# Optimization experiments

Measured on AMD Instinct MI355X. Metric: run time of the kernel, lower is better.

Reference implementation:

```python
import jax, jax.numpy as jnp
import numpy as np


def setup_inputs() -> dict:
    key = jax.random.key(0)
    ks = jax.random.split(key, 6)
    b, t, s, qu, vu, d = 8, 64, 512, 512, 512, 512
    return {
        "query": jax.random.normal(ks[0], (b, t, qu), jnp.float32),
        "value": jax.random.normal(ks[1], (b, s, vu), jnp.float32),
        "mask": jax.random.randint(ks[2], (b, s), 0, 2).astype(bool),
        "W1_w": jax.random.normal(ks[3], (qu, d), jnp.float32) * (1.0 / np.sqrt(qu)),
        "W1_b": jnp.zeros((d,), jnp.float32),
        "W2_w": jax.random.normal(ks[4], (vu, d), jnp.float32) * (1.0 / np.sqrt(vu)),
        "W2_b": jnp.zeros((d,), jnp.float32),
        "scale": jax.random.normal(ks[5], (d,), jnp.float32) * 0.05,
    }


def reference(query, value, mask, W1_w, W1_b, W2_w, W2_b, scale):
    # Dense projections
    q = jnp.einsum('btq,qd->btd', query, W1_w) + W1_b   # [b,t,d]
    k = jnp.einsum('bsv,vd->bsd', value, W2_w) + W2_b   # [b,s,d]
    # Additive (Bahdanau) score with learned scale vector (Keras use_scale=True)
    # scores[b,t,s] = sum_d scale[d] * tanh(q[b,t,d] + k[b,s,d])
    scores = jnp.einsum('btsd,d->bts', jnp.tanh(q[:, :, None, :] + k[:, None, :, :]), scale)
    # Mask over source positions (value mask); query mask is all-ones (no-op)
    scores = jnp.where(mask[:, None, :], scores, jnp.float32(-1e9))
    attention_weights = jax.nn.softmax(scores, axis=-1)   # [b,t,s]
    context_vector = jnp.einsum('bts,bsv->btv', attention_weights, value)  # [b,t,vu]
    return context_vector, attention_weights
```

## Files before the change

kernel.cpp:

```cpp
#include <hip/hip_runtime.h>
#include <hip/hip_bf16.h>

#define B_  8
#define T_  64
#define S_  512
#define D_  512

#define QN (512 * 512)
#define KN (4096 * 512)

#define TLOG2E 2.8853900817779268f
#define LOG2E  1.4426950408889634f

typedef __attribute__((ext_vector_type(8))) short bf16x8;
typedef __attribute__((ext_vector_type(4))) float f32x4;

__device__ __forceinline__ unsigned int pk2(float a, float b) {
    float2 f; f.x = a; f.y = b;
    __hip_bfloat162 h = __float22bfloat162_rn(f);
    return *(unsigned int*)&h;
}
#define BF2X(U) __uint_as_float((U) << 16)
#define BF2Y(U) __uint_as_float((U) & 0xffff0000u)

__global__ __launch_bounds__(256) void mfma_gemm(
    const float* __restrict__ query, const float* __restrict__ value,
    const float* __restrict__ W1, const float* __restrict__ W2,
    const float* __restrict__ b1, const float* __restrict__ b2,
    float* __restrict__ qproj, unsigned short* __restrict__ kTb)
{
    __shared__ __align__(16) unsigned short Ab[2][64][72];
    __shared__ __align__(16) unsigned short Bs[2][64][72];

    const int x = blockIdx.x;
    const float *A, *W;
    int tm, tn;
    bool isq;
    if (x < 512) {
        tm = (x & 7) * 8 + ((x >> 3) & 7);
        tn = x >> 6;
        A = value; W = W2; isq = false;
    } else {
        int r = x - 512;
        tm = r >> 3; tn = r & 7;
        A = query; W = W1; isq = true;
    }

    const int tid  = threadIdx.x;
    const int lane = tid & 63;
    const int wid  = tid >> 6;
    const int wm = (wid & 1) * 32, wn = (wid >> 1) * 32;
    const int fm = lane & 15, fq = lane >> 4;

    f32x4 acc00 = {0.f, 0.f, 0.f, 0.f};
    f32x4 acc01 = acc00, acc10 = acc00, acc11 = acc00;

    const int ar = tid >> 2;
    const int kc = (tid & 3) * 16;
    const float* Ag = A + (size_t)(tm * 64 + ar) * 512 + kc;
    const int c0 = (tid & 15) * 4;
    const int kp = (tid >> 4) * 2;
    const float* Wg = W + (size_t)kp * 512 + tn * 64 + c0;

    float4 av0, av1, av2, av3;
    float4 wv0, wv1, wv2, wv3;

#define LOADT(KOFF) do {                                                      \
        av0 = *(const float4*)(Ag + (KOFF));                                  \
        av1 = *(const float4*)(Ag + (KOFF) + 4);                              \
        av2 = *(const float4*)(Ag + (KOFF) + 8);                              \
        av3 = *(const float4*)(Ag + (KOFF) + 12);                             \
        wv0 = *(const float4*)(Wg + (size_t)(KOFF) * 512);                    \
        wv1 = *(const float4*)(Wg + (size_t)(KOFF) * 512 + 512);              \
        wv2 = *(const float4*)(Wg + (size_t)((KOFF) + 32) * 512);             \
        wv3 = *(const float4*)(Wg + (size_t)((KOFF) + 32) * 512 + 512);       \
    } while (0)

#define STAGE(BUF) do {                                                       \
        uint4 p0, p1;                                                         \
        p0.x = pk2(av0.x, av0.y); p0.y = pk2(av0.z, av0.w);                   \
        p0.z = pk2(av1.x, av1.y); p0.w = pk2(av1.z, av1.w);                   \
        p1.x = pk2(av2.x, av2.y); p1.y = pk2(av2.z, av2.w);                   \
        p1.z = pk2(av3.x, av3.y); p1.w = pk2(av3.z, av3.w);                   \
        *(uint4*)&Ab[BUF][ar][kc]     = p0;                                   \
        *(uint4*)&Ab[BUF][ar][kc + 8] = p1;                                   \
        *(unsigned int*)&Bs[BUF][c0 + 0][kp]      = pk2(wv0.x, wv1.x);        \
        *(unsigned int*)&Bs[BUF][c0 + 1][kp]      = pk2(wv0.y, wv1.y);        \
        *(unsigned int*)&Bs[BUF][c0 + 2][kp]      = pk2(wv0.z, wv1.z);        \
        *(unsigned int*)&Bs[BUF][c0 + 3][kp]      = pk2(wv0.w, wv1.w);        \
        *(unsigned int*)&Bs[BUF][c0 + 0][kp + 32] = pk2(wv2.x, wv3.x);        \
        *(unsigned int*)&Bs[BUF][c0 + 1][kp + 32] = pk2(wv2.y, wv3.y);        \
        *(unsigned int*)&Bs[BUF][c0 + 2][kp + 32] = pk2(wv2.z, wv3.z);        \
        *(unsigned int*)&Bs[BUF][c0 + 3][kp + 32] = pk2(wv2.w, wv3.w);        \
    } while (0)

    LOADT(0);
    STAGE(0);
    LOADT(64);
    __syncthreads();

    for (int i = 0; i < 8; ++i) {
        const int cur = i & 1, nxt = cur ^ 1;
        bf16x8 a0, a1, b0, b1v;
#pragma unroll
        for (int kk = 0; kk < 64; kk += 32) {
            a0  = *(const bf16x8*)&Ab[cur][wm + fm][kk + fq * 8];
            a1  = *(const bf16x8*)&Ab[cur][wm + 16 + fm][kk + fq * 8];
            b0  = *(const bf16x8*)&Bs[cur][wn + fm][kk + fq * 8];
            b1v = *(const bf16x8*)&Bs[cur][wn + 16 + fm][kk + fq * 8];
            acc00 = __builtin_amdgcn_mfma_f32_16x16x32_bf16(a0, b0,  acc00, 0, 0, 0);
            acc01 = __builtin_amdgcn_mfma_f32_16x16x32_bf16(a0, b1v, acc01, 0, 0, 0);
            acc10 = __builtin_amdgcn_mfma_f32_16x16x32_bf16(a1, b0,  acc10, 0, 0, 0);
            acc11 = __builtin_amdgcn_mfma_f32_16x16x32_bf16(a1, b1v, acc11, 0, 0, 0);
        }
        if (i < 7) {
            STAGE(nxt);
            const int kn = ((i + 2) & 7) * 64;
            LOADT(kn);
        }
        __syncthreads();
    }
#undef STAGE
#undef LOADT

    const int n0 = tn * 64 + wn + fm;
    const int n1 = n0 + 16;
    const int m0 = tm * 64 + wm + fq * 4;
    if (isq) {
        float bias0 = b1[n0] + b2[n0];
        float bias1 = b1[n1] + b2[n1];
#pragma unroll
        for (int r = 0; r < 4; ++r) {
            qproj[(size_t)(m0 + r) * 512 + n0]      = (acc00[r] + bias0) * TLOG2E;
            qproj[(size_t)(m0 + r) * 512 + n1]      = (acc01[r] + bias1) * TLOG2E;
            qproj[(size_t)(m0 + 16 + r) * 512 + n0] = (acc10[r] + bias0) * TLOG2E;
            qproj[(size_t)(m0 + 16 + r) * 512 + n1] = (acc11[r] + bias1) * TLOG2E;
        }
    } else {
        const int bb = m0 >> 9;
        const int sl = m0 & 511;
        unsigned short* kb = kTb + (size_t)(bb * 512) * 512;
        uint2 o;
        o.x = pk2(acc00[0] * TLOG2E, acc00[1] * TLOG2E);
        o.y = pk2(acc00[2] * TLOG2E, acc00[3] * TLOG2E);
        *(uint2*)(kb + (size_t)n0 * 512 + sl) = o;
        o.x = pk2(acc10[0] * TLOG2E, acc10[1] * TLOG2E);
        o.y = pk2(acc10[2] * TLOG2E, acc10[3] * TLOG2E);
        *(uint2*)(kb + (size_t)n0 * 512 + sl + 16) = o;
        o.x = pk2(acc01[0] * TLOG2E, acc01[1] * TLOG2E);
        o.y = pk2(acc01[2] * TLOG2E, acc01[3] * TLOG2E);
        *(uint2*)(kb + (size_t)n1 * 512 + sl) = o;
        o.x = pk2(acc11[0] * TLOG2E, acc11[1] * TLOG2E);
        o.y = pk2(acc11[2] * TLOG2E, acc11[3] * TLOG2E);
        *(uint2*)(kb + (size_t)n1 * 512 + sl + 16) = o;
    }
}

__global__ __launch_bounds__(1024) void fused_attn(
    const float* __restrict__ qproj, const unsigned short* __restrict__ kTb,
    const int*   __restrict__ mask,  const float* __restrict__ scale,
    const float* __restrict__ value,
    float* __restrict__ ctx, float* __restrict__ attn)
{
    const int blk = blockIdx.x;
    const int b  = blk & 7;
    const int tp = blk >> 3;
    const size_t row0 = (size_t)(b * T_ + tp * 2);

    __shared__ __align__(16) float q0A[512];
    __shared__ __align__(16) float dA[512];
    __shared__ __align__(16) float cA[512];
    __shared__ __align__(16) float4 pex[4][256];
    __shared__ __align__(16) float2 wp2[512];
    __shared__ __align__(16) float4 part[2][8][128];
    __shared__ float2 red2[16];

    const int tid  = threadIdx.x;
    const int lane = tid & 63;
    const int wid  = tid >> 6;

    if (tid < 512) {
        float q0v = qproj[row0 * D_ + tid];
        float q1v = qproj[(row0 + 1) * D_ + tid];
        q0A[tid] = q0v;
        dA[tid]  = __builtin_amdgcn_exp2f(q1v - q0v);
        cA[tid]  = scale[tid];
    }
    __syncthreads();

    const int sp  = tid & 255;
    const int dq  = tid >> 8;
    const int dlo = dq * 128;
    const unsigned short* kb = kTb + ((size_t)(b * 512 + dlo)) * 512 + sp * 2;

    float p00 = 0.f, p10 = 0.f, p01 = 0.f, p11 = 0.f;

    unsigned int nf0 = *(const unsigned int*)(kb);
    unsigned int nf1 = *(const unsigned int*)(kb + 512);
    unsigned int nf2 = *(const unsigned int*)(kb + 1024);
    unsigned int nf3 = *(const unsigned int*)(kb + 1536);

#define SC2(KU, QV, DV, CV) do {                                              \
        float e0 = __builtin_amdgcn_exp2f((QV) + BF2X(KU));                   \
        float ra = __builtin_amdgcn_rcpf(e0 + 1.0f);                          \
        float rb = __builtin_amdgcn_rcpf(fmaf(e0, (DV), 1.0f));               \
        p00 = fmaf((CV), ra, p00); p10 = fmaf((CV), rb, p10);                 \
        float e1 = __builtin_amdgcn_exp2f((QV) + BF2Y(KU));                   \
        float rc = __builtin_amdgcn_rcpf(e1 + 1.0f);                          \
        float rd = __builtin_amdgcn_rcpf(fmaf(e1, (DV), 1.0f));               \
        p01 = fmaf((CV), rc, p01); p11 = fmaf((CV), rd, p11);                 \
    } while (0)

    for (int g = 0; g < 32; ++g) {
        unsigned int kf0 = nf0, kf1 = nf1, kf2 = nf2, kf3 = nf3;
        const unsigned short* nb = kb + (size_t)(((g + 1) & 31) * 4) * 512;
        nf0 = *(const unsigned int*)(nb);
        nf1 = *(const unsigned int*)(nb + 512);
        nf2 = *(const unsigned int*)(nb + 1024);
        nf3 = *(const unsigned int*)(nb + 1536);
        const int d0 = dlo + g * 4;
        float4 q4 = *(const float4*)&q0A[d0];
        float4 dl = *(const float4*)&dA[d0];
        float4 c4 = *(const float4*)&cA[d0];
        SC2(kf0, q4.x, dl.x, c4.x);
        SC2(kf1, q4.y, dl.y, c4.y);
        SC2(kf2, q4.z, dl.z, c4.z);
        SC2(kf3, q4.w, dl.w, c4.w);
    }
#undef SC2

    {
        float4 pq; pq.x = p00; pq.y = p10; pq.z = p01; pq.w = p11;
        pex[dq][sp] = pq;
    }
    __syncthreads();

    float x0 = 0.f, x1 = 0.f;
    if (tid < 512) {
        const int s = tid;
        const int s2 = s >> 1;
        const bool odd = (s & 1) != 0;
        float4 r0 = pex[0][s2], r1 = pex[1][s2];
        float4 r2 = pex[2][s2], r3 = pex[3][s2];
        float pt0 = odd ? ((r0.z + r1.z) + (r2.z + r3.z))
                        : ((r0.x + r1.x) + (r2.x + r3.x));
        float pt1 = odd ? ((r0.w + r1.w) + (r2.w + r3.w))
                        : ((r0.y + r1.y) + (r2.y + r3.y));
        const int m = mask[b * S_ + s];
        x0 = m ? (-2.0f * pt0) : -1e9f;
        x1 = m ? (-2.0f * pt1) : -1e9f;
        float2 mx; mx.x = x0; mx.y = x1;
#pragma unroll
        for (int off = 32; off >= 1; off >>= 1) {
            mx.x = fmaxf(mx.x, __shfl_xor(mx.x, off));
            mx.y = fmaxf(mx.y, __shfl_xor(mx.y, off));
        }
        if (lane == 0) red2[wid] = mx;
    }
    __syncthreads();

    float e0 = 0.f, e1 = 0.f;
    if (tid < 512) {
        float2 M = red2[0];
#pragma unroll
        for (int i = 1; i < 8; ++i) {
            M.x = fmaxf(M.x, red2[i].x);
            M.y = fmaxf(M.y, red2[i].y);
        }
        e0 = __builtin_amdgcn_exp2f((x0 - M.x) * LOG2E);
        e1 = __builtin_amdgcn_exp2f((x1 - M.y) * LOG2E);
        float2 sm; sm.x = e0; sm.y = e1;
#pragma unroll
        for (int off = 32; off >= 1; off >>= 1) {
            sm.x += __shfl_xor(sm.x, off);
            sm.y += __shfl_xor(sm.y, off);
        }
        if (lane == 0) red2[8 + wid] = sm;
    }
    __syncthreads();

    if (tid < 512) {
        const int s = tid;
        float2 SS = red2[8];
#pragma unroll
        for (int i = 9; i < 16; ++i) {
            SS.x += red2[i].x;
            SS.y += red2[i].y;
        }
        const float w0 = e0 * __builtin_amdgcn_rcpf(SS.x);
        const float w1 = e1 * __builtin_amdgcn_rcpf(SS.y);
        float2 wpair; wpair.x = w0; wpair.y = w1;
        wp2[s] = wpair;
        attn[row0 * S_ + s]       = w0;
        attn[(row0 + 1) * S_ + s] = w1;
    }
    __syncthreads();

    const int g  = tid >> 7;
    const int v4 = tid & 127;
    const float* vb = value + ((size_t)(b * S_) + g * 64) * D_ + v4 * 4;
    float4 a0; a0.x = 0.f; a0.y = 0.f; a0.z = 0.f; a0.w = 0.f;
    float4 a1 = a0;
#pragma unroll 4
    for (int i = 0; i < 64; ++i) {
        float4 vv = *(const float4*)(vb + (size_t)i * D_);
        float2 w = wp2[g * 64 + i];
        a0.x = fmaf(w.x, vv.x, a0.x); a0.y = fmaf(w.x, vv.y, a0.y);
        a0.z = fmaf(w.x, vv.z, a0.z); a0.w = fmaf(w.x, vv.w, a0.w);
        a1.x = fmaf(w.y, vv.x, a1.x); a1.y = fmaf(w.y, vv.y, a1.y);
        a1.z = fmaf(w.y, vv.z, a1.z); a1.w = fmaf(w.y, vv.w, a1.w);
    }
    part[0][g][v4] = a0;
    part[1][g][v4] = a1;
    __syncthreads();
    if (tid < 256) {
        const int t = tid >> 7, v = tid & 127;
        float4 o; o.x = 0.f; o.y = 0.f; o.z = 0.f; o.w = 0.f;
#pragma unroll
        for (int gg = 0; gg < 8; ++gg) {
            float4 p = part[t][gg][v];
            o.x += p.x; o.y += p.y; o.z += p.z; o.w += p.w;
        }
        *(float4*)(ctx + (row0 + t) * D_ + v * 4) = o;
    }
}

extern "C" void kernel_launch(void* const* d_in, const int* in_sizes, int n_in,
                              void* d_out, int out_size, void* d_ws, size_t ws_size,
                              hipStream_t stream) {
    const float* query = (const float*)d_in[0];
    const float* value = (const float*)d_in[1];
    const int*   mask  = (const int*)  d_in[2];
    const float* W1w   = (const float*)d_in[3];
    const float* W1b   = (const float*)d_in[4];
    const float* W2w   = (const float*)d_in[5];
    const float* W2b   = (const float*)d_in[6];
    const float* scale = (const float*)d_in[7];

    float* ctx  = (float*)d_out;
    float* attn = (float*)d_out + (size_t)B_ * T_ * D_;

    float* qproj = (float*)d_ws;
    unsigned short* kTb = (unsigned short*)(qproj + (size_t)QN);

    mfma_gemm<<<576, 256, 0, stream>>>(query, value, W1w, W2w, W1b, W2b,
                                       qproj, kTb);
    fused_attn<<<256, 1024, 0, stream>>>(qproj, kTb, mask, scale, value,
                                         ctx, attn);
}
```

Baseline: 126.3 us.

## Merge projection GEMM and attention into one persistent kernel with grid barrier

```diff
diff --git a/kernel.cpp b/kernel.cpp
--- a/kernel.cpp
+++ b/kernel.cpp
@@ -23,182 +23,177 @@
 #define BF2X(U) __uint_as_float((U) << 16)
 #define BF2Y(U) __uint_as_float((U) & 0xffff0000u)
 
-__global__ __launch_bounds__(256) void mfma_gemm(
+__global__ __launch_bounds__(1024, 4) void mega(
     const float* __restrict__ query, const float* __restrict__ value,
     const float* __restrict__ W1, const float* __restrict__ W2,
     const float* __restrict__ b1, const float* __restrict__ b2,
-    float* __restrict__ qproj, unsigned short* __restrict__ kTb)
-{
-    __shared__ __align__(16) unsigned short Ab[2][64][72];
-    __shared__ __align__(16) unsigned short Bs[2][64][72];
-
-    const int x = blockIdx.x;
-    const float *A, *W;
-    int tm, tn;
-    bool isq;
-    if (x < 512) {
-        tm = (x & 7) * 8 + ((x >> 3) & 7);
-        tn = x >> 6;
-        A = value; W = W2; isq = false;
-    } else {
-        int r = x - 512;
-        tm = r >> 3; tn = r & 7;
-        A = query; W = W1; isq = true;
-    }
-
-    const int tid  = threadIdx.x;
-    const int lane = tid & 63;
-    const int wid  = tid >> 6;
-    const int wm = (wid & 1) * 32, wn = (wid >> 1) * 32;
-    const int fm = lane & 15, fq = lane >> 4;
-
-    f32x4 acc00 = {0.f, 0.f, 0.f, 0.f};
-    f32x4 acc01 = acc00, acc10 = acc00, acc11 = acc00;
-
-    const int ar = tid >> 2;
-    const int kc = (tid & 3) * 16;
-    const float* Ag = A + (size_t)(tm * 64 + ar) * 512 + kc;
-    const int c0 = (tid & 15) * 4;
-    const int kp = (tid >> 4) * 2;
-    const float* Wg = W + (size_t)kp * 512 + tn * 64 + c0;
-
-    float4 av0, av1, av2, av3;
-    float4 wv0, wv1, wv2, wv3;
-
-#define LOADT(KOFF) do {                                                      \
-        av0 = *(const float4*)(Ag + (KOFF));                                  \
-        av1 = *(const float4*)(Ag + (KOFF) + 4);                              \
-        av2 = *(const float4*)(Ag + (KOFF) + 8);                              \
-        av3 = *(const float4*)(Ag + (KOFF) + 12);                             \
-        wv0 = *(const float4*)(Wg + (size_t)(KOFF) * 512);                    \
-        wv1 = *(const float4*)(Wg + (size_t)(KOFF) * 512 + 512);              \
-        wv2 = *(const float4*)(Wg + (size_t)((KOFF) + 32) * 512);             \
-        wv3 = *(const float4*)(Wg + (size_t)((KOFF) + 32) * 512 + 512);       \
-    } while (0)
-
-#define STAGE(BUF) do {                                                       \
-        uint4 p0, p1;                                                         \
-        p0.x = pk2(av0.x, av0.y); p0.y = pk2(av0.z, av0.w);                   \
-        p0.z = pk2(av1.x, av1.y); p0.w = pk2(av1.z, av1.w);                   \
-        p1.x = pk2(av2.x, av2.y); p1.y = pk2(av2.z, av2.w);                   \
-        p1.z = pk2(av3.x, av3.y); p1.w = pk2(av3.z, av3.w);                   \
-        *(uint4*)&Ab[BUF][ar][kc]     = p0;                                   \
-        *(uint4*)&Ab[BUF][ar][kc + 8] = p1;                                   \
-        *(unsigned int*)&Bs[BUF][c0 + 0][kp]      = pk2(wv0.x, wv1.x);        \
-        *(unsigned int*)&Bs[BUF][c0 + 1][kp]      = pk2(wv0.y, wv1.y);        \
-        *(unsigned int*)&Bs[BUF][c0 + 2][kp]      = pk2(wv0.z, wv1.z);        \
-        *(unsigned int*)&Bs[BUF][c0 + 3][kp]      = pk2(wv0.w, wv1.w);        \
-        *(unsigned int*)&Bs[BUF][c0 + 0][kp + 32] = pk2(wv2.x, wv3.x);        \
-        *(unsigned int*)&Bs[BUF][c0 + 1][kp + 32] = pk2(wv2.y, wv3.y);        \
-        *(unsigned int*)&Bs[BUF][c0 + 2][kp + 32] = pk2(wv2.z, wv3.z);        \
-        *(unsigned int*)&Bs[BUF][c0 + 3][kp + 32] = pk2(wv2.w, wv3.w);        \
-    } while (0)
-
-    LOADT(0);
-    STAGE(0);
-    LOADT(64);
-    __syncthreads();
-
-    for (int i = 0; i < 8; ++i) {
-        const int cur = i & 1, nxt = cur ^ 1;
-        bf16x8 a0, a1, b0, b1v;
-#pragma unroll
-        for (int kk = 0; kk < 64; kk += 32) {
-            a0  = *(const bf16x8*)&Ab[cur][wm + fm][kk + fq * 8];
-            a1  = *(const bf16x8*)&Ab[cur][wm + 16 + fm][kk + fq * 8];
-            b0  = *(const bf16x8*)&Bs[cur][wn + fm][kk + fq * 8];
-            b1v = *(const bf16x8*)&Bs[cur][wn + 16 + fm][kk + fq * 8];
-            acc00 = __builtin_amdgcn_mfma_f32_16x16x32_bf16(a0, b0,  acc00, 0, 0, 0);
-            acc01 = __builtin_amdgcn_mfma_f32_16x16x32_bf16(a0, b1v, acc01, 0, 0, 0);
-            acc10 = __builtin_amdgcn_mfma_f32_16x16x32_bf16(a1, b0,  acc10, 0, 0, 0);
-            acc11 = __builtin_amdgcn_mfma_f32_16x16x32_bf16(a1, b1v, acc11, 0, 0, 0);
-        }
-        if (i < 7) {
-            STAGE(nxt);
-            const int kn = ((i + 2) & 7) * 64;
-            LOADT(kn);
-        }
-        __syncthreads();
-    }
-#undef STAGE
-#undef LOADT
-
-    const int n0 = tn * 64 + wn + fm;
-    const int n1 = n0 + 16;
-    const int m0 = tm * 64 + wm + fq * 4;
-    if (isq) {
-        float bias0 = b1[n0] + b2[n0];
-        float bias1 = b1[n1] + b2[n1];
-#pragma unroll
-        for (int r = 0; r < 4; ++r) {
-            qproj[(size_t)(m0 + r) * 512 + n0]      = (acc00[r] + bias0) * TLOG2E;
-            qproj[(size_t)(m0 + r) * 512 + n1]      = (acc01[r] + bias1) * TLOG2E;
-            qproj[(size_t)(m0 + 16 + r) * 512 + n0] = (acc10[r] + bias0) * TLOG2E;
-            qproj[(size_t)(m0 + 16 + r) * 512 + n1] = (acc11[r] + bias1) * TLOG2E;
-        }
-    } else {
-        const int bb = m0 >> 9;
-        const int sl = m0 & 511;
-        unsigned short* kb = kTb + (size_t)(bb * 512) * 512;
-        uint2 o;
-        o.x = pk2(acc00[0] * TLOG2E, acc00[1] * TLOG2E);
-        o.y = pk2(acc00[2] * TLOG2E, acc00[3] * TLOG2E);
-        *(uint2*)(kb + (size_t)n0 * 512 + sl) = o;
-        o.x = pk2(acc10[0] * TLOG2E, acc10[1] * TLOG2E);
-        o.y = pk2(acc10[2] * TLOG2E, acc10[3] * TLOG2E);
-        *(uint2*)(kb + (size_t)n0 * 512 + sl + 16) = o;
-        o.x = pk2(acc01[0] * TLOG2E, acc01[1] * TLOG2E);
-        o.y = pk2(acc01[2] * TLOG2E, acc01[3] * TLOG2E);
-        *(uint2*)(kb + (size_t)n1 * 512 + sl) = o;
-        o.x = pk2(acc11[0] * TLOG2E, acc11[1] * TLOG2E);
-        o.y = pk2(acc11[2] * TLOG2E, acc11[3] * TLOG2E);
-        *(uint2*)(kb + (size_t)n1 * 512 + sl + 16) = o;
-    }
-}
-
-__global__ __launch_bounds__(1024) void fused_attn(
-    const float* __restrict__ qproj, const unsigned short* __restrict__ kTb,
-    const int*   __restrict__ mask,  const float* __restrict__ scale,
-    const float* __restrict__ value,
+    const int*  __restrict__ mask, const float* __restrict__ scale,
+    float* __restrict__ qproj, unsigned short* __restrict__ kTb,
+    unsigned int* __restrict__ ctr,
     float* __restrict__ ctx, float* __restrict__ attn)
 {
+    __shared__ __align__(16) char smem[59520];
+
+    const int tid = threadIdx.x;
     const int blk = blockIdx.x;
-    const int b  = blk & 7;
-    const int tp = blk >> 3;
-    const size_t row0 = (size_t)(b * T_ + tp * 2);
-
-    __shared__ __align__(16) float q0A[512];
-    __shared__ __align__(16) float dA[512];
-    __shared__ __align__(16) float cA[512];
-    __shared__ __align__(16) float4 pex[4][256];
-    __shared__ __align__(16) float2 wp2[512];
-    __shared__ __align__(16) float4 part[2][8][128];
-    __shared__ float2 red2[16];
-
-    const int tid  = threadIdx.x;
-    const int lane = tid & 63;
-    const int wid  = tid >> 6;
-
-    if (tid < 512) {
-        float q0v = qproj[row0 * D_ + tid];
-        float q1v = qproj[(row0 + 1) * D_ + tid];
-        q0A[tid] = q0v;
-        dA[tid]  = __builtin_amdgcn_exp2f(q1v - q0v);
-        cA[tid]  = scale[tid];
+    const int x = blk & 7;
+    const int r = blk >> 3;
+
+    {
+        const int team = tid >> 8;
+        const int ttid = tid & 255;
+
+        int kind = 0, tmt = 0, tnt = 0;
+        if (r < 16)       { kind = 1; int l = r * 4 + team; tmt = x * 8 + (l >> 3); tnt = l & 7; }
+        else if (r == 16) { kind = 2; tmt = x; tnt = team; }
+        else if (r == 17) { kind = 2; tmt = x; tnt = 4 + team; }
+
+        const float* A = (kind == 2) ? query : value;
+        const float* W = (kind == 2) ? W1 : W2;
+
+        unsigned short (*Ab)[40] = (unsigned short(*)[40])(smem + team * 10240);
+        unsigned short (*Bs)[40] = (unsigned short(*)[40])(smem + team * 10240 + 5120);
+
+        const int twid = ttid >> 6;
+        const int lane = ttid & 63;
+        const int wm = (twid & 1) * 32, wn = (twid >> 1) * 32;
+        const int fm = lane & 15, fq = lane >> 4;
+
+        f32x4 acc00 = {0.f, 0.f, 0.f, 0.f};
+        f32x4 acc01 = acc00, acc10 = acc00, acc11 = acc00;
+
+        const int ar = ttid >> 2;
+        const int ac = (ttid & 3) * 8;
+        const float* Ag = A + (size_t)(tmt * 64 + ar) * 512 + ac;
+        const int c0 = (ttid & 15) * 4;
+        const int kp = (ttid >> 4) * 2;
+        const float* Wg = W + (size_t)kp * 512 + tnt * 64 + c0;
+
+        float4 av0, av1, wv0, wv1;
+        if (kind) {
+            av0 = *(const float4*)(Ag);
+            av1 = *(const float4*)(Ag + 4);
+            wv0 = *(const float4*)(Wg);
+            wv1 = *(const float4*)(Wg + 512);
+        }
+
+        for (int i = 0; i < 16; ++i) {
+            if (kind) {
+                uint4 pa;
+                pa.x = pk2(av0.x, av0.y); pa.y = pk2(av0.z, av0.w);
+                pa.z = pk2(av1.x, av1.y); pa.w = pk2(av1.z, av1.w);
+                *(uint4*)&Ab[ar][ac] = pa;
+                *(unsigned int*)&Bs[c0 + 0][kp] = pk2(wv0.x, wv1.x);
+                *(unsigned int*)&Bs[c0 + 1][kp] = pk2(wv0.y, wv1.y);
+                *(unsigned int*)&Bs[c0 + 2][kp] = pk2(wv0.z, wv1.z);
+                *(unsigned int*)&Bs[c0 + 3][kp] = pk2(wv0.w, wv1.w);
+            }
+            __syncthreads();
+            if (kind) {
+                bf16x8 a0  = *(const bf16x8*)&Ab[wm + fm][fq * 8];
+                bf16x8 a1  = *(const bf16x8*)&Ab[wm + 16 + fm][fq * 8];
+                bf16x8 b0  = *(const bf16x8*)&Bs[wn + fm][fq * 8];
+                bf16x8 b1v = *(const bf16x8*)&Bs[wn + 16 + fm][fq * 8];
+                if (i < 15) {
+                    const int kn = (i + 1) * 32;
+                    av0 = *(const float4*)(Ag + kn);
+                    av1 = *(const float4*)(Ag + kn + 4);
+                    wv0 = *(const float4*)(Wg + (size_t)kn * 512);
+                    wv1 = *(const float4*)(Wg + (size_t)kn * 512 + 512);
+                }
+                acc00 = __builtin_amdgcn_mfma_f32_16x16x32_bf16(a0, b0,  acc00, 0, 0, 0);
+                acc01 = __builtin_amdgcn_mfma_f32_16x16x32_bf16(a0, b1v, acc01, 0, 0, 0);
+                acc10 = __builtin_amdgcn_mfma_f32_16x16x32_bf16(a1, b0,  acc10, 0, 0, 0);
+                acc11 = __builtin_amdgcn_mfma_f32_16x16x32_bf16(a1, b1v, acc11, 0, 0, 0);
+            }
+            __syncthreads();
+        }
+
+        if (kind == 2) {
+            const int n0 = tnt * 64 + wn + fm;
+            const int n1 = n0 + 16;
+            const int m0 = tmt * 64 + wm + fq * 4;
+            float bias0 = b1[n0] + b2[n0];
+            float bias1 = b1[n1] + b2[n1];
+#pragma unroll
+            for (int rr = 0; rr < 4; ++rr) {
+                qproj[(size_t)(m0 + rr) * 512 + n0]      = (acc00[rr] + bias0) * TLOG2E;
+                qproj[(size_t)(m0 + rr) * 512 + n1]      = (acc01[rr] + bias1) * TLOG2E;
+                qproj[(size_t)(m0 + 16 + rr) * 512 + n0] = (acc10[rr] + bias0) * TLOG2E;
+                qproj[(size_t)(m0 + 16 + rr) * 512 + n1] = (acc11[rr] + bias1) * TLOG2E;
+            }
+        } else if (kind == 1) {
+            const int n0 = tnt * 64 + wn + fm;
+            const int n1 = n0 + 16;
+            const int m0 = tmt * 64 + wm + fq * 4;
+            const int bb = m0 >> 9;
+            const int sl = m0 & 511;
+            unsigned short* kb = kTb + (size_t)(bb * 512) * 512;
+            uint2 o;
+            o.x = pk2(acc00[0] * TLOG2E, acc00[1] * TLOG2E);
+            o.y = pk2(acc00[2] * TLOG2E, acc00[3] * TLOG2E);
+            *(uint2*)(kb + (size_t)n0 * 512 + sl) = o;
+            o.x = pk2(acc10[0] * TLOG2E, acc10[1] * TLOG2E);
+            o.y = pk2(acc10[2] * TLOG2E, acc10[3] * TLOG2E);
+            *(uint2*)(kb + (size_t)n0 * 512 + sl + 16) = o;
+            o.x = pk2(acc01[0] * TLOG2E, acc01[1] * TLOG2E);
+            o.y = pk2(acc01[2] * TLOG2E, acc01[3] * TLOG2E);
+            *(uint2*)(kb + (size_t)n1 * 512 + sl) = o;
+            o.x = pk2(acc11[0] * TLOG2E, acc11[1] * TLOG2E);
+            o.y = pk2(acc11[2] * TLOG2E, acc11[3] * TLOG2E);
+            *(uint2*)(kb + (size_t)n1 * 512 + sl + 16) = o;
+        }
+    }
+
+    __syncthreads();
+    if (tid == 0) {
+        __threadfence();
+        __hip_atomic_fetch_add(ctr, 1u, __ATOMIC_RELEASE, __HIP_MEMORY_SCOPE_AGENT);
+        unsigned int v; unsigned long it = 0;
+        do {
+            v = __hip_atomic_load(ctr, __ATOMIC_ACQUIRE, __HIP_MEMORY_SCOPE_AGENT);
+            if (v >= 256u) break;
+            __builtin_amdgcn_s_sleep(2);
+        } while (++it < 100000000ul);
     }
     __syncthreads();
 
-    const int sp  = tid & 255;
-    const int dq  = tid >> 8;
-    const int dlo = dq * 128;
-    const unsigned short* kb = kTb + ((size_t)(b * 512 + dlo)) * 512 + sp * 2;
-
-    float p00 = 0.f, p10 = 0.f, p01 = 0.f, p11 = 0.f;
-
-    unsigned int nf0 = *(const unsigned int*)(kb);
-    unsigned int nf1 = *(const unsigned int*)(kb + 512);
-    unsigned int nf2 = *(const unsigned int*)(kb + 1024);
-    unsigned int nf3 = *(const unsigned int*)(kb + 1536);
+    {
+        const int b  = x;
+        const int tp = r;
+        const size_t row0 = (size_t)(b * T_ + tp * 2);
+
+        float*  q0A = (float*)(smem);
+        float*  dA  = (float*)(smem + 2048);
+        float*  cA  = (float*)(smem + 4096);
+        float4 (*pex)[256]      = (float4(*)[256])(smem + 6144);
+        float2* wp2 = (float2*)(smem + 22528);
+        float4 (*part)[8][128]  = (float4(*)[8][128])(smem + 26624);
+        float2* red2 = (float2*)(smem + 59392);
+
+        const int lane = tid & 63;
+        const int wid  = tid >> 6;
+
+        if (tid < 512) {
+            float q0v = qproj[row0 * D_ + tid];
+            float q1v = qproj[(row0 + 1) * D_ + tid];
+            q0A[tid] = q0v;
+            dA[tid]  = __builtin_amdgcn_exp2f(q1v - q0v);
+            cA[tid]  = scale[tid];
+        }
+        __syncthreads();
+
+        const int sp  = tid & 255;
+        const int dq  = tid >> 8;
+        const int dlo = dq * 128;
+        const unsigned short* kb = kTb + ((size_t)(b * 512 + dlo)) * 512 + sp * 2;
+
+        float p00 = 0.f, p10 = 0.f, p01 = 0.f, p11 = 0.f;
+
+        unsigned int nf0 = *(const unsigned int*)(kb);
+        unsigned int nf1 = *(const unsigned int*)(kb + 512);
+        unsigned int nf2 = *(const unsigned int*)(kb + 1024);
+        unsigned int nf3 = *(const unsigned int*)(kb + 1536);
 
 #define SC2(KU, QV, DV, CV) do {                                              \
         float e0 = __builtin_amdgcn_exp2f((QV) + BF2X(KU));                   \
@@ -211,117 +206,118 @@
         p01 = fmaf((CV), rc, p01); p11 = fmaf((CV), rd, p11);                 \
     } while (0)
 
-    for (int g = 0; g < 32; ++g) {
-        unsigned int kf0 = nf0, kf1 = nf1, kf2 = nf2, kf3 = nf3;
-        const unsigned short* nb = kb + (size_t)(((g + 1) & 31) * 4) * 512;
-        nf0 = *(const unsigned int*)(nb);
-        nf1 = *(const unsigned int*)(nb + 512);
-        nf2 = *(const unsigned int*)(nb + 1024);
-        nf3 = *(const unsigned int*)(nb + 1536);
-        const int d0 = dlo + g * 4;
-        float4 q4 = *(const float4*)&q0A[d0];
-        float4 dl = *(const float4*)&dA[d0];
-        float4 c4 = *(const float4*)&cA[d0];
-        SC2(kf0, q4.x, dl.x, c4.x);
-        SC2(kf1, q4.y, dl.y, c4.y);
-        SC2(kf2, q4.z, dl.z, c4.z);
-        SC2(kf3, q4.w, dl.w, c4.w);
-    }
+        for (int g = 0; g < 32; ++g) {
+            unsigned int kf0 = nf0, kf1 = nf1, kf2 = nf2, kf3 = nf3;
+            const unsigned short* nb = kb + (size_t)(((g + 1) & 31) * 4) * 512;
+            nf0 = *(const unsigned int*)(nb);
+            nf1 = *(const unsigned int*)(nb + 512);
+            nf2 = *(const unsigned int*)(nb + 1024);
+            nf3 = *(const unsigned int*)(nb + 1536);
+            const int d0 = dlo + g * 4;
+            float4 q4 = *(const float4*)&q0A[d0];
+            float4 dl = *(const float4*)&dA[d0];
+            float4 c4 = *(const float4*)&cA[d0];
+            SC2(kf0, q4.x, dl.x, c4.x);
+            SC2(kf1, q4.y, dl.y, c4.y);
+            SC2(kf2, q4.z, dl.z, c4.z);
+            SC2(kf3, q4.w, dl.w, c4.w);
+        }
 #undef SC2
 
-    {
-        float4 pq; pq.x = p00; pq.y = p10; pq.z = p01; pq.w = p11;
-        pex[dq][sp] = pq;
-    }
-    __syncthreads();
-
-    float x0 = 0.f, x1 = 0.f;
-    if (tid < 512) {
-        const int s = tid;
-        const int s2 = s >> 1;
-        const bool odd = (s & 1) != 0;
-        float4 r0 = pex[0][s2], r1 = pex[1][s2];
-        float4 r2 = pex[2][s2], r3 = pex[3][s2];
-        float pt0 = odd ? ((r0.z + r1.z) + (r2.z + r3.z))
-                        : ((r0.x + r1.x) + (r2.x + r3.x));
-        float pt1 = odd ? ((r0.w + r1.w) + (r2.w + r3.w))
-                        : ((r0.y + r1.y) + (r2.y + r3.y));
-        const int m = mask[b * S_ + s];
-        x0 = m ? (-2.0f * pt0) : -1e9f;
-        x1 = m ? (-2.0f * pt1) : -1e9f;
-        float2 mx; mx.x = x0; mx.y = x1;
-#pragma unroll
-        for (int off = 32; off >= 1; off >>= 1) {
-            mx.x = fmaxf(mx.x, __shfl_xor(mx.x, off));
-            mx.y = fmaxf(mx.y, __shfl_xor(mx.y, off));
-        }
-        if (lane == 0) red2[wid] = mx;
-    }
-    __syncthreads();
-
-    float e0 = 0.f, e1 = 0.f;
-    if (tid < 512) {
-        float2 M = red2[0];
-#pragma unroll
-        for (int i = 1; i < 8; ++i) {
-            M.x = fmaxf(M.x, red2[i].x);
-            M.y = fmaxf(M.y, red2[i].y);
-        }
-        e0 = __builtin_amdgcn_exp2f((x0 - M.x) * LOG2E);
-        e1 = __builtin_amdgcn_exp2f((x1 - M.y) * LOG2E);
-        float2 sm; sm.x = e0; sm.y = e1;
-#pragma unroll
-        for (int off = 32; off >= 1; off >>= 1) {
-            sm.x += __shfl_xor(sm.x, off);
-            sm.y += __shfl_xor(sm.y, off);
-        }
-        if (lane == 0) red2[8 + wid] = sm;
-    }
-    __syncthreads();
-
-    if (tid < 512) {
-        const int s = tid;
-        float2 SS = red2[8];
-#pragma unroll
-        for (int i = 9; i < 16; ++i) {
-            SS.x += red2[i].x;
-            SS.y += red2[i].y;
-        }
-        const float w0 = e0 * __builtin_amdgcn_rcpf(SS.x);
-        const float w1 = e1 * __builtin_amdgcn_rcpf(SS.y);
-        float2 wpair; wpair.x = w0; wpair.y = w1;
-        wp2[s] = wpair;
-        attn[row0 * S_ + s]       = w0;
-        attn[(row0 + 1) * S_ + s] = w1;
-    }
-    __syncthreads();
-
-    const int g  = tid >> 7;
-    const int v4 = tid & 127;
-    const float* vb = value + ((size_t)(b * S_) + g * 64) * D_ + v4 * 4;
-    float4 a0; a0.x = 0.f; a0.y = 0.f; a0.z = 0.f; a0.w = 0.f;
-    float4 a1 = a0;
+        {
+            float4 pq; pq.x = p00; pq.y = p10; pq.z = p01; pq.w = p11;
+            pex[dq][sp] = pq;
+        }
+        __syncthreads();
+
+        float x0 = 0.f, x1 = 0.f;
+        if (tid < 512) {
+            const int s = tid;
+            const int s2 = s >> 1;
+            const bool odd = (s & 1) != 0;
+            float4 r0 = pex[0][s2], r1 = pex[1][s2];
+            float4 r2 = pex[2][s2], r3 = pex[3][s2];
+            float pt0 = odd ? ((r0.z + r1.z) + (r2.z + r3.z))
+                            : ((r0.x + r1.x) + (r2.x + r3.x));
+            float pt1 = odd ? ((r0.w + r1.w) + (r2.w + r3.w))
+                            : ((r0.y + r1.y) + (r2.y + r3.y));
+            const int m = mask[b * S_ + s];
+            x0 = m ? (-2.0f * pt0) : -1e9f;
+            x1 = m ? (-2.0f * pt1) : -1e9f;
+            float2 mx; mx.x = x0; mx.y = x1;
+#pragma unroll
+            for (int off = 32; off >= 1; off >>= 1) {
+                mx.x = fmaxf(mx.x, __shfl_xor(mx.x, off));
+                mx.y = fmaxf(mx.y, __shfl_xor(mx.y, off));
+            }
+            if (lane == 0) red2[wid] = mx;
+        }
+        __syncthreads();
+
+        float e0 = 0.f, e1 = 0.f;
+        if (tid < 512) {
+            float2 M = red2[0];
+#pragma unroll
+            for (int i = 1; i < 8; ++i) {
+                M.x = fmaxf(M.x, red2[i].x);
+                M.y = fmaxf(M.y, red2[i].y);
+            }
+            e0 = __builtin_amdgcn_exp2f((x0 - M.x) * LOG2E);
+            e1 = __builtin_amdgcn_exp2f((x1 - M.y) * LOG2E);
+            float2 sm; sm.x = e0; sm.y = e1;
+#pragma unroll
+            for (int off = 32; off >= 1; off >>= 1) {
+                sm.x += __shfl_xor(sm.x, off);
+                sm.y += __shfl_xor(sm.y, off);
+            }
+            if (lane == 0) red2[8 + wid] = sm;
+        }
+        __syncthreads();
+
+        if (tid < 512) {
+            const int s = tid;
+            float2 SS = red2[8];
+#pragma unroll
+            for (int i = 9; i < 16; ++i) {
+                SS.x += red2[i].x;
+                SS.y += red2[i].y;
+            }
+            const float w0 = e0 * __builtin_amdgcn_rcpf(SS.x);
+            const float w1 = e1 * __builtin_amdgcn_rcpf(SS.y);
+            float2 wpair; wpair.x = w0; wpair.y = w1;
+            wp2[s] = wpair;
+            attn[row0 * S_ + s]       = w0;
+            attn[(row0 + 1) * S_ + s] = w1;
+        }
+        __syncthreads();
+
+        const int g  = tid >> 7;
+        const int v4 = tid & 127;
+        const float* vb = value + ((size_t)(b * S_) + g * 64) * D_ + v4 * 4;
+        float4 a0; a0.x = 0.f; a0.y = 0.f; a0.z = 0.f; a0.w = 0.f;
+        float4 a1 = a0;
 #pragma unroll 4
-    for (int i = 0; i < 64; ++i) {
-        float4 vv = *(const float4*)(vb + (size_t)i * D_);
-        float2 w = wp2[g * 64 + i];
-        a0.x = fmaf(w.x, vv.x, a0.x); a0.y = fmaf(w.x, vv.y, a0.y);
-        a0.z = fmaf(w.x, vv.z, a0.z); a0.w = fmaf(w.x, vv.w, a0.w);
-        a1.x = fmaf(w.y, vv.x, a1.x); a1.y = fmaf(w.y, vv.y, a1.y);
-        a1.z = fmaf(w.y, vv.z, a1.z); a1.w = fmaf(w.y, vv.w, a1.w);
-    }
-    part[0][g][v4] = a0;
-    part[1][g][v4] = a1;
-    __syncthreads();
-    if (tid < 256) {
-        const int t = tid >> 7, v = tid & 127;
-        float4 o; o.x = 0.f; o.y = 0.f; o.z = 0.f; o.w = 0.f;
-#pragma unroll
-        for (int gg = 0; gg < 8; ++gg) {
-            float4 p = part[t][gg][v];
-            o.x += p.x; o.y += p.y; o.z += p.z; o.w += p.w;
-        }
-        *(float4*)(ctx + (row0 + t) * D_ + v * 4) = o;
+        for (int i = 0; i < 64; ++i) {
+            float4 vv = *(const float4*)(vb + (size_t)i * D_);
+            float2 w = wp2[g * 64 + i];
+            a0.x = fmaf(w.x, vv.x, a0.x); a0.y = fmaf(w.x, vv.y, a0.y);
+            a0.z = fmaf(w.x, vv.z, a0.z); a0.w = fmaf(w.x, vv.w, a0.w);
+            a1.x = fmaf(w.y, vv.x, a1.x); a1.y = fmaf(w.y, vv.y, a1.y);
+            a1.z = fmaf(w.y, vv.z, a1.z); a1.w = fmaf(w.y, vv.w, a1.w);
+        }
+        part[0][g][v4] = a0;
+        part[1][g][v4] = a1;
+        __syncthreads();
+        if (tid < 256) {
+            const int t = tid >> 7, v = tid & 127;
+            float4 o; o.x = 0.f; o.y = 0.f; o.z = 0.f; o.w = 0.f;
+#pragma unroll
+            for (int gg = 0; gg < 8; ++gg) {
+                float4 p = part[t][gg][v];
+                o.x += p.x; o.y += p.y; o.z += p.z; o.w += p.w;
+            }
+            *(float4*)(ctx + (row0 + t) * D_ + v * 4) = o;
+        }
     }
 }
 
@@ -342,9 +338,9 @@
 
     float* qproj = (float*)d_ws;
     unsigned short* kTb = (unsigned short*)(qproj + (size_t)QN);
-
-    mfma_gemm<<<576, 256, 0, stream>>>(query, value, W1w, W2w, W1b, W2b,
-                                       qproj, kTb);
-    fused_attn<<<256, 1024, 0, stream>>>(qproj, kTb, mask, scale, value,
-                                         ctx, attn);
+    unsigned int* ctr = (unsigned int*)((char*)d_ws + (6u << 20));
+
+    hipMemsetAsync(ctr, 0, 4, stream);
+    mega<<<256, 1024, 0, stream>>>(query, value, W1w, W2w, W1b, W2b,
+                                   mask, scale, qproj, kTb, ctr, ctx, attn);
 }
```

New measurement: 193.8 us. 1.53x slower.
